# Performance work log

Hardware: AMD Instinct MI355X
Metric: run time of the kernel (lower is better)

The kernel has to match this reference:

```python
import jax, jax.numpy as jnp
import numpy as np

B, S, D, H = 4, 2048, 1024, 16
HD = D // H

def setup_inputs() -> dict:
    key = jax.random.key(0)
    ks = jax.random.split(key, 5)
    x = jax.random.normal(ks[0], (B, S, D), dtype=jnp.float32)
    mask = jnp.ones((B, S), dtype=jnp.int32)
    # torch nn.Linear init scale ~ 1/sqrt(fan_in); use small normal for stability
    qkv_w = jax.random.normal(ks[1], (3 * D, D), dtype=jnp.float32) * (1.0 / np.sqrt(D))
    qkv_b = jax.random.normal(ks[2], (3 * D,), dtype=jnp.float32) * 0.02
    out_w = jax.random.normal(ks[3], (D, D), dtype=jnp.float32) * (1.0 / np.sqrt(D))
    out_b = jax.random.normal(ks[4], (D,), dtype=jnp.float32) * 0.02
    return {"x": x, "mask": mask, "qkv_w": qkv_w, "qkv_b": qkv_b,
            "out_w": out_w, "out_b": out_b}

def reference(x, mask, qkv_w, qkv_b, out_w, out_b):
    b, s, d = x.shape
    scale = np.sqrt(HD).astype(np.float32)
    # qkv projection: torch Linear y = x @ W^T + b
    qkv = x @ qkv_w.T + qkv_b                      # (b, s, 3d)
    qkv = qkv.reshape(b, s, 3, H, HD)
    qkv = jnp.transpose(qkv, (2, 0, 3, 1, 4))      # (3, b, H, s, hd)
    q, k, v = qkv[0], qkv[1], qkv[2]
    scores = jnp.einsum('bhqd,bhkd->bhqk', q, k) / scale  # (b, H, s, s)
    neg_inf = jnp.float32(-jnp.inf)
    causal = jnp.tril(jnp.ones((s, s), dtype=bool))
    scores = jnp.where(causal[None, None], scores, neg_inf)
    key_mask = (mask != 0)[:, None, None, :]       # (b, 1, 1, s)
    scores = jnp.where(key_mask, scores, neg_inf)
    attn = jax.nn.softmax(scores, axis=-1)
    out = jnp.einsum('bhqk,bhkd->bhqd', attn, v)   # (b, H, s, hd)
    out = jnp.transpose(out, (0, 2, 1, 3)).reshape(b, s, d)
    return out @ out_w.T + out_b
```

## Files before the change

### kernel.cpp

```cpp
#include <hip/hip_runtime.h>
#include <stdint.h>
#include <type_traits>

#define BB  4
#define SS  2048
#define DD  1024
#define HH  16
#define HDD 64

typedef __attribute__((ext_vector_type(8))) short s16x8;
typedef __attribute__((ext_vector_type(4))) float f32x4;

__device__ inline short f2bf(float f) {
    union { float f; unsigned int u; } v; v.f = f;
    unsigned int r = (v.u + 0x7fffu + ((v.u >> 16) & 1u)) >> 16;
    return (short)r;
}

__device__ inline float bf2f(short s) {
    union { unsigned int u; float f; } v;
    v.u = ((unsigned int)(unsigned short)s) << 16;
    return v.f;
}

#define GLL(gp, lp) __builtin_amdgcn_global_load_lds( \
    (const __attribute__((address_space(1))) void*)(gp), \
    (__attribute__((address_space(3))) void*)(lp), 16, 0, 0)

__device__ inline void lds_barrier() {
    asm volatile("s_waitcnt lgkmcnt(0)" ::: "memory");
    __builtin_amdgcn_sched_barrier(0);
    __builtin_amdgcn_s_barrier();
    __builtin_amdgcn_sched_barrier(0);
}

__global__ void cvt_kernel(const float* __restrict__ src, short* __restrict__ dst, int n) {
    int i = (blockIdx.x * 256 + threadIdx.x) * 8;
    if (i >= n) return;
    const float4* s = (const float4*)(src + i);
    float4 a = s[0], b = s[1];
    s16x8 o;
    o[0]=f2bf(a.x); o[1]=f2bf(a.y); o[2]=f2bf(a.z); o[3]=f2bf(a.w);
    o[4]=f2bf(b.x); o[5]=f2bf(b.y); o[6]=f2bf(b.z); o[7]=f2bf(b.w);
    *(s16x8*)(dst + i) = o;
}

template<int EPI>
__global__ __launch_bounds__(256)
void gemm_bt(const short* __restrict__ A, const short* __restrict__ Bw,
             const float* __restrict__ bias, float* __restrict__ Cf,
             short* __restrict__ Qo, short* __restrict__ Ko, short* __restrict__ Vo,
             int M, int N, int K)
{
    __shared__ short lsA[128 * 32];
    __shared__ short lsB[128 * 32];
    const int tid  = threadIdx.x;
    const int w    = tid >> 6, lane = tid & 63;
    const int quad = lane >> 4, l15 = lane & 15;
    const int m0 = blockIdx.x * 128, n0 = blockIdx.y * 128;
    const int mw = (w & 1) * 64, nw = (w >> 1) * 64;

    f32x4 acc[4][4] = {};

    const int srow = w * 32 + (lane >> 2);
    const int scol = (lane & 3) * 8;
    const short* pA = A + (size_t)(m0 + srow) * K + scol;
    const short* pB = Bw + (size_t)(n0 + srow) * K + scol;
    short* lAbase0 = &lsA[(w * 32) * 32];
    short* lAbase1 = &lsA[(w * 32 + 16) * 32];
    short* lBbase0 = &lsB[(w * 32) * 32];
    short* lBbase1 = &lsB[(w * 32 + 16) * 32];

    for (int kk = 0; kk < K; kk += 32) {
        __syncthreads();
        GLL(pA + kk,            lAbase0);
        GLL(pA + kk + 16 * K,   lAbase1);
        GLL(pB + kk,            lBbase0);
        GLL(pB + kk + 16 * K,   lBbase1);
        asm volatile("s_waitcnt vmcnt(0)" ::: "memory");
        __syncthreads();

        s16x8 af[4], bfr[4];
        for (int t = 0; t < 4; ++t) {
            af[t]  = *(const s16x8*)&lsA[(mw + t * 16 + l15) * 32 + quad * 8];
            bfr[t] = *(const s16x8*)&lsB[(nw + t * 16 + l15) * 32 + quad * 8];
        }
        for (int i = 0; i < 4; ++i)
            for (int j = 0; j < 4; ++j)
                acc[i][j] = __builtin_amdgcn_mfma_f32_16x16x32_bf16(af[i], bfr[j], acc[i][j], 0, 0, 0);
    }

    if (EPI == 0) {
        for (int i = 0; i < 4; ++i) {
            int row = m0 + mw + i * 16 + quad * 4;
            for (int j = 0; j < 4; ++j) {
                int col = n0 + nw + j * 16 + l15;
                float bv = bias[col];
                for (int r = 0; r < 4; ++r)
                    Cf[(size_t)(row + r) * N + col] = acc[i][j][r] + bv;
            }
        }
    } else {
        for (int i = 0; i < 4; ++i) {
            int row = m0 + mw + i * 16 + quad * 4;
            for (int j = 0; j < 4; ++j) {
                int col = n0 + nw + j * 16 + l15;
                float bv = bias[col];
                int sel = col >> 10, h = (col >> 6) & 15, hd = col & 63;
                for (int r = 0; r < 4; ++r) {
                    int rr = row + r;
                    int b = rr >> 11, s = rr & 2047;
                    short val = f2bf(acc[i][j][r] + bv);
                    if (sel == 0)      Qo[(((size_t)b * HH + h) * SS + s) * HDD + hd] = val;
                    else if (sel == 1) Ko[(((size_t)b * HH + h) * SS + s) * HDD + hd] = val;
                    else               Vo[(((size_t)b * HH + h) * HDD + hd) * SS + s] = val;
                }
            }
        }
    }
}

__global__ __launch_bounds__(256, 4)
void attn_kernel(const short* __restrict__ Q, const short* __restrict__ Kb,
                 const short* __restrict__ Vb, const int* __restrict__ mask,
                 short* __restrict__ O)
{
    __shared__ short lsK[2][64 * 64];
    __shared__ short lsV[2][64 * 64];
    __shared__ short lsM[SS];

    const int tid  = threadIdx.x;
    const int w    = tid >> 6, lane = tid & 63;
    const int quad = lane >> 4, l15 = lane & 15;
    const int bx = blockIdx.x, bh = blockIdx.y;
    const int b = bh >> 4;
    const size_t baseQK = (size_t)bh * SS * HDD;
    const size_t baseV  = (size_t)bh * HDD * SS;
    const float SC = 0.18033688f;
    const int grow = lane >> 3;
    const int gcol = ((lane & 7) ^ grow) * 8;
    const int l7 = l15 & 7;

    {
        const int4* mp = (const int4*)(mask + b * SS);
        int4 a = mp[tid * 2], c = mp[tid * 2 + 1];
        const short NEG = f2bf(-1e30f);
        s16x8 mo;
        mo[0] = a.x ? (short)0 : NEG; mo[1] = a.y ? (short)0 : NEG;
        mo[2] = a.z ? (short)0 : NEG; mo[3] = a.w ? (short)0 : NEG;
        mo[4] = c.x ? (short)0 : NEG; mo[5] = c.y ? (short)0 : NEG;
        mo[6] = c.z ? (short)0 : NEG; mo[7] = c.w ? (short)0 : NEG;
        *(s16x8*)&lsM[tid * 8] = mo;
    }

    auto issue = [&](int kv0, int buf) {
#pragma unroll
        for (int jj = 0; jj < 2; ++jj) {
            int row = w * 16 + jj * 8 + grow;
            GLL(Kb + baseQK + (size_t)(kv0 + row) * HDD + gcol,
                &lsK[buf][(w * 2 + jj) * 512]);
        }
#pragma unroll
        for (int jj = 0; jj < 2; ++jj) {
            int row = w * 16 + jj * 8 + grow;
            GLL(Vb + baseV + (size_t)row * SS + kv0 + gcol,
                &lsV[buf][(w * 2 + jj) * 512]);
        }
    };

    for (int t = 0; t < 2; ++t) {
        const int qb = t ? bx : (31 - bx);
        const int q0 = qb * 64;
        const int qrow = q0 + w * 16 + l15;
        const int rowg0 = q0 + w * 16 + quad * 4;

        s16x8 aq[2];
#pragma unroll
        for (int ks = 0; ks < 2; ++ks)
            aq[ks] = *(const s16x8*)(Q + baseQK + (size_t)qrow * HDD + ks * 32 + quad * 8);

        float m_r[4], l_r[4];
        f32x4 o_acc[4] = {};
#pragma unroll
        for (int r = 0; r < 4; ++r) { m_r[r] = -1e30f; l_r[r] = 0.f; }

        const int ntiles = qb + 1;

        lds_barrier();
        issue(0, 0);

        auto tile = [&](auto CC, int kv0, int buf, int kvn) {
            constexpr bool CAUS = decltype(CC)::value;

            lds_barrier();
            if (kvn >= 0) issue(kvn, buf ^ 1);

            float madd[4];
#pragma unroll
            for (int nt = 0; nt < 4; ++nt)
                madd[nt] = bf2f(lsM[kv0 + nt * 16 + l15]);

            if (kvn >= 0) asm volatile("s_waitcnt vmcnt(4)" ::: "memory");
            else          asm volatile("s_waitcnt vmcnt(0)" ::: "memory");
            __builtin_amdgcn_sched_barrier(0);
            __builtin_amdgcn_s_barrier();
            __builtin_amdgcn_sched_barrier(0);

            f32x4 sv[4];
#pragma unroll
            for (int nt = 0; nt < 4; ++nt) sv[nt] = f32x4{};
#pragma unroll
            for (int ks = 0; ks < 2; ++ks)
#pragma unroll
                for (int nt = 0; nt < 4; ++nt) {
                    s16x8 kf = *(const s16x8*)&lsK[buf][(nt * 16 + l15) * 64 +
                                                       (((ks * 4 + quad) ^ l7) * 8)];
                    sv[nt] = __builtin_amdgcn_mfma_f32_16x16x32_bf16(aq[ks], kf, sv[nt], 0, 0, 0);
                }

#pragma unroll
            for (int nt = 0; nt < 4; ++nt) {
                int colg = kv0 + nt * 16 + l15;
#pragma unroll
                for (int r = 0; r < 4; ++r) {
                    float scv = sv[nt][r] * SC + madd[nt];
                    if (CAUS && colg > rowg0 + r) scv = -1e30f;
                    sv[nt][r] = scv;
                }
            }
            float alpha[4];
#pragma unroll
            for (int r = 0; r < 4; ++r) {
                float rm = fmaxf(fmaxf(sv[0][r], sv[1][r]), fmaxf(sv[2][r], sv[3][r]));
                rm = fmaxf(rm, __shfl_xor(rm, 1));
                rm = fmaxf(rm, __shfl_xor(rm, 2));
                rm = fmaxf(rm, __shfl_xor(rm, 4));
                rm = fmaxf(rm, __shfl_xor(rm, 8));
                float nm = fmaxf(m_r[r], rm);
                alpha[r] = __builtin_amdgcn_exp2f(m_r[r] - nm);
                m_r[r] = nm;
                float rs = 0.f;
#pragma unroll
                for (int nt = 0; nt < 4; ++nt) {
                    float p = __builtin_amdgcn_exp2f(sv[nt][r] - nm);
                    sv[nt][r] = p;
                    rs += p;
                }
                rs += __shfl_xor(rs, 1);
                rs += __shfl_xor(rs, 2);
                rs += __shfl_xor(rs, 4);
                rs += __shfl_xor(rs, 8);
                l_r[r] = l_r[r] * alpha[r] + rs;
            }
#pragma unroll
            for (int ht = 0; ht < 4; ++ht)
#pragma unroll
                for (int r = 0; r < 4; ++r)
                    o_acc[ht][r] *= alpha[r];

            lds_barrier();

            short* lsPw = &lsK[buf][w * 1024];
#pragma unroll
            for (int nt = 0; nt < 4; ++nt)
#pragma unroll
                for (int r = 0; r < 4; ++r) {
                    int prow = quad * 4 + r;
                    lsPw[prow * 64 + (((nt * 2 + (l15 >> 3)) ^ (prow & 7)) << 3) + l7]
                        = f2bf(sv[nt][r]);
                }
            asm volatile("s_waitcnt lgkmcnt(0)" ::: "memory");
            __builtin_amdgcn_sched_barrier(0);

            s16x8 ap[2];
#pragma unroll
            for (int k2 = 0; k2 < 2; ++k2)
                ap[k2] = *(const s16x8*)&lsPw[l15 * 64 + (((k2 * 4 + quad) ^ l7) << 3)];
#pragma unroll
            for (int ht = 0; ht < 4; ++ht)
#pragma unroll
                for (int k2 = 0; k2 < 2; ++k2) {
                    s16x8 vf = *(const s16x8*)&lsV[buf][(ht * 16 + l15) * 64 +
                                                        (((k2 * 4 + quad) ^ l7) * 8)];
                    o_acc[ht] = __builtin_amdgcn_mfma_f32_16x16x32_bf16(ap[k2], vf, o_acc[ht], 0, 0, 0);
                }
        };

        for (int kt = 0; kt < ntiles; ++kt) {
            const int kvn = (kt + 1 < ntiles) ? (kt + 1) * 64 : -1;
            if (kt == ntiles - 1) tile(std::true_type{},  kt * 64, kt & 1, kvn);
            else                  tile(std::false_type{}, kt * 64, kt & 1, kvn);
        }

        const int hcol = (bh & 15) * HDD;
#pragma unroll
        for (int r = 0; r < 4; ++r) {
            float inv = 1.0f / l_r[r];
            int srow = q0 + w * 16 + quad * 4 + r;
            size_t base = ((size_t)b * SS + srow) * DD + hcol;
#pragma unroll
            for (int ht = 0; ht < 4; ++ht)
                O[base + ht * 16 + l15] = f2bf(o_acc[ht][r] * inv);
        }
    }
}

extern "C" void kernel_launch(void* const* d_in, const int* in_sizes, int n_in,
                              void* d_out, int out_size, void* d_ws, size_t ws_size,
                              hipStream_t stream) {
    const float* x     = (const float*)d_in[0];
    const int*   mask  = (const int*)d_in[1];
    const float* qkv_w = (const float*)d_in[2];
    const float* qkv_b = (const float*)d_in[3];
    const float* out_w = (const float*)d_in[4];
    const float* out_b = (const float*)d_in[5];
    float* out = (float*)d_out;

    const size_t M1 = (size_t)BB * SS;
    short* ws  = (short*)d_ws;
    short* xb  = ws;
    short* qwb = xb  + M1 * DD;
    short* owb = qwb + (size_t)3 * DD * DD;
    short* Qb  = owb + (size_t)DD * DD;
    short* Kb  = Qb  + M1 * DD;
    short* Vb  = Kb  + M1 * DD;
    short* Ob  = Vb  + M1 * DD;

    cvt_kernel<<<(int)(M1 * DD / 8 / 256), 256, 0, stream>>>(x, xb, (int)(M1 * DD));
    cvt_kernel<<<3 * DD * DD / 8 / 256, 256, 0, stream>>>(qkv_w, qwb, 3 * DD * DD);
    cvt_kernel<<<DD * DD / 8 / 256, 256, 0, stream>>>(out_w, owb, DD * DD);

    gemm_bt<1><<<dim3(64, 24), 256, 0, stream>>>(xb, qwb, qkv_b, nullptr,
                                                 Qb, Kb, Vb, 8192, 3072, 1024);
    attn_kernel<<<dim3(16, BB * HH), 256, 0, stream>>>(Qb, Kb, Vb, mask, Ob);
    gemm_bt<0><<<dim3(64, 8), 256, 0, stream>>>(Ob, owb, out_b, out,
                                                nullptr, nullptr, nullptr, 8192, 1024, 1024);
}
```

Baseline: 350.7 us.

## Enlarge attention query tile to 128 rows with lazy softmax rescaling

```diff
diff --git a/kernel.cpp b/kernel.cpp
--- a/kernel.cpp
+++ b/kernel.cpp
@@ -120,13 +120,14 @@
     }
 }
 
-__global__ __launch_bounds__(256, 4)
+__global__ __launch_bounds__(256, 2)
 void attn_kernel(const short* __restrict__ Q, const short* __restrict__ Kb,
                  const short* __restrict__ Vb, const int* __restrict__ mask,
                  short* __restrict__ O)
 {
     __shared__ short lsK[2][64 * 64];
     __shared__ short lsV[2][64 * 64];
+    __shared__ short lsP[4][32 * 64];
     __shared__ short lsM[SS];
 
     const int tid  = threadIdx.x;
@@ -169,22 +170,26 @@
     };
 
     for (int t = 0; t < 2; ++t) {
-        const int qb = t ? bx : (31 - bx);
-        const int q0 = qb * 64;
-        const int qrow = q0 + w * 16 + l15;
-        const int rowg0 = q0 + w * 16 + quad * 4;
-
-        s16x8 aq[2];
-#pragma unroll
-        for (int ks = 0; ks < 2; ++ks)
-            aq[ks] = *(const s16x8*)(Q + baseQK + (size_t)qrow * HDD + ks * 32 + quad * 8);
-
-        float m_r[4], l_r[4];
-        f32x4 o_acc[4] = {};
-#pragma unroll
-        for (int r = 0; r < 4; ++r) { m_r[r] = -1e30f; l_r[r] = 0.f; }
-
-        const int ntiles = qb + 1;
+        const int qb = t ? bx : (15 - bx);
+        const int q0 = qb * 128;
+        const int qw0 = q0 + w * 32;
+
+        s16x8 aq[2][2];
+#pragma unroll
+        for (int s = 0; s < 2; ++s)
+#pragma unroll
+            for (int ks = 0; ks < 2; ++ks)
+                aq[s][ks] = *(const s16x8*)(Q + baseQK +
+                    (size_t)(qw0 + s * 16 + l15) * HDD + ks * 32 + quad * 8);
+
+        float m_r[2][4], l_r[2][4];
+        f32x4 o_acc[2][4] = {};
+#pragma unroll
+        for (int s = 0; s < 2; ++s)
+#pragma unroll
+            for (int r = 0; r < 4; ++r) { m_r[s][r] = -1e30f; l_r[s][r] = 0.f; }
+
+        const int ntiles = 2 * qb + 2;
 
         lds_barrier();
         issue(0, 0);
@@ -206,102 +211,142 @@
             __builtin_amdgcn_s_barrier();
             __builtin_amdgcn_sched_barrier(0);
 
-            f32x4 sv[4];
-#pragma unroll
-            for (int nt = 0; nt < 4; ++nt) sv[nt] = f32x4{};
+            f32x4 sv[2][4];
+#pragma unroll
+            for (int s = 0; s < 2; ++s)
+#pragma unroll
+                for (int nt = 0; nt < 4; ++nt) sv[s][nt] = f32x4{};
 #pragma unroll
             for (int ks = 0; ks < 2; ++ks)
 #pragma unroll
                 for (int nt = 0; nt < 4; ++nt) {
                     s16x8 kf = *(const s16x8*)&lsK[buf][(nt * 16 + l15) * 64 +
                                                        (((ks * 4 + quad) ^ l7) * 8)];
-                    sv[nt] = __builtin_amdgcn_mfma_f32_16x16x32_bf16(aq[ks], kf, sv[nt], 0, 0, 0);
-                }
-
-#pragma unroll
-            for (int nt = 0; nt < 4; ++nt) {
-                int colg = kv0 + nt * 16 + l15;
+#pragma unroll
+                    for (int s = 0; s < 2; ++s)
+                        sv[s][nt] = __builtin_amdgcn_mfma_f32_16x16x32_bf16(
+                                        aq[s][ks], kf, sv[s][nt], 0, 0, 0);
+                }
+
+#pragma unroll
+            for (int s = 0; s < 2; ++s) {
+                const int rowg0 = qw0 + s * 16 + quad * 4;
+#pragma unroll
+                for (int nt = 0; nt < 4; ++nt) {
+                    int colg = kv0 + nt * 16 + l15;
+#pragma unroll
+                    for (int r = 0; r < 4; ++r) {
+                        float scv = sv[s][nt][r] * SC + madd[nt];
+                        if (CAUS && colg > rowg0 + r) scv = -1e30f;
+                        sv[s][nt][r] = scv;
+                    }
+                }
+            }
+
+            float rm[2][4];
+#pragma unroll
+            for (int s = 0; s < 2; ++s)
 #pragma unroll
                 for (int r = 0; r < 4; ++r) {
-                    float scv = sv[nt][r] * SC + madd[nt];
-                    if (CAUS && colg > rowg0 + r) scv = -1e30f;
-                    sv[nt][r] = scv;
-                }
-            }
-            float alpha[4];
-#pragma unroll
-            for (int r = 0; r < 4; ++r) {
-                float rm = fmaxf(fmaxf(sv[0][r], sv[1][r]), fmaxf(sv[2][r], sv[3][r]));
-                rm = fmaxf(rm, __shfl_xor(rm, 1));
-                rm = fmaxf(rm, __shfl_xor(rm, 2));
-                rm = fmaxf(rm, __shfl_xor(rm, 4));
-                rm = fmaxf(rm, __shfl_xor(rm, 8));
-                float nm = fmaxf(m_r[r], rm);
-                alpha[r] = __builtin_amdgcn_exp2f(m_r[r] - nm);
-                m_r[r] = nm;
-                float rs = 0.f;
-#pragma unroll
-                for (int nt = 0; nt < 4; ++nt) {
-                    float p = __builtin_amdgcn_exp2f(sv[nt][r] - nm);
-                    sv[nt][r] = p;
-                    rs += p;
-                }
-                rs += __shfl_xor(rs, 1);
-                rs += __shfl_xor(rs, 2);
-                rs += __shfl_xor(rs, 4);
-                rs += __shfl_xor(rs, 8);
-                l_r[r] = l_r[r] * alpha[r] + rs;
-            }
-#pragma unroll
-            for (int ht = 0; ht < 4; ++ht)
+                    float v = fmaxf(fmaxf(sv[s][0][r], sv[s][1][r]),
+                                    fmaxf(sv[s][2][r], sv[s][3][r]));
+                    v = fmaxf(v, __shfl_xor(v, 1));
+                    v = fmaxf(v, __shfl_xor(v, 2));
+                    v = fmaxf(v, __shfl_xor(v, 4));
+                    v = fmaxf(v, __shfl_xor(v, 8));
+                    rm[s][r] = v;
+                }
+            float need = rm[0][0] - m_r[0][0];
+#pragma unroll
+            for (int s = 0; s < 2; ++s)
 #pragma unroll
                 for (int r = 0; r < 4; ++r)
-                    o_acc[ht][r] *= alpha[r];
-
-            lds_barrier();
-
-            short* lsPw = &lsK[buf][w * 1024];
-#pragma unroll
-            for (int nt = 0; nt < 4; ++nt)
+                    need = fmaxf(need, rm[s][r] - m_r[s][r]);
+            if (!__all(need <= 8.0f)) {
+#pragma unroll
+                for (int s = 0; s < 2; ++s)
+#pragma unroll
+                    for (int r = 0; r < 4; ++r) {
+                        float nm = fmaxf(m_r[s][r], rm[s][r]);
+                        float al = __builtin_amdgcn_exp2f(m_r[s][r] - nm);
+                        m_r[s][r] = nm;
+                        l_r[s][r] *= al;
+#pragma unroll
+                        for (int ht = 0; ht < 4; ++ht)
+                            o_acc[s][ht][r] *= al;
+                    }
+            }
+#pragma unroll
+            for (int s = 0; s < 2; ++s)
 #pragma unroll
                 for (int r = 0; r < 4; ++r) {
-                    int prow = quad * 4 + r;
-                    lsPw[prow * 64 + (((nt * 2 + (l15 >> 3)) ^ (prow & 7)) << 3) + l7]
-                        = f2bf(sv[nt][r]);
-                }
+                    float rs = 0.f;
+#pragma unroll
+                    for (int nt = 0; nt < 4; ++nt) {
+                        float p = __builtin_amdgcn_exp2f(sv[s][nt][r] - m_r[s][r]);
+                        sv[s][nt][r] = p;
+                        rs += p;
+                    }
+                    l_r[s][r] += rs;
+                }
+
+            short* lsPw = lsP[w];
+#pragma unroll
+            for (int s = 0; s < 2; ++s)
+#pragma unroll
+                for (int nt = 0; nt < 4; ++nt)
+#pragma unroll
+                    for (int r = 0; r < 4; ++r) {
+                        int prow = s * 16 + quad * 4 + r;
+                        lsPw[prow * 64 + (((nt * 2 + (l15 >> 3)) ^ (prow & 7)) << 3) + l7]
+                            = f2bf(sv[s][nt][r]);
+                    }
             asm volatile("s_waitcnt lgkmcnt(0)" ::: "memory");
             __builtin_amdgcn_sched_barrier(0);
 
-            s16x8 ap[2];
-#pragma unroll
-            for (int k2 = 0; k2 < 2; ++k2)
-                ap[k2] = *(const s16x8*)&lsPw[l15 * 64 + (((k2 * 4 + quad) ^ l7) << 3)];
+            s16x8 ap[2][2];
+#pragma unroll
+            for (int s = 0; s < 2; ++s)
+#pragma unroll
+                for (int k2 = 0; k2 < 2; ++k2)
+                    ap[s][k2] = *(const s16x8*)&lsPw[(s * 16 + l15) * 64 +
+                                                     (((k2 * 4 + quad) ^ l7) << 3)];
 #pragma unroll
             for (int ht = 0; ht < 4; ++ht)
 #pragma unroll
                 for (int k2 = 0; k2 < 2; ++k2) {
                     s16x8 vf = *(const s16x8*)&lsV[buf][(ht * 16 + l15) * 64 +
                                                         (((k2 * 4 + quad) ^ l7) * 8)];
-                    o_acc[ht] = __builtin_amdgcn_mfma_f32_16x16x32_bf16(ap[k2], vf, o_acc[ht], 0, 0, 0);
+#pragma unroll
+                    for (int s = 0; s < 2; ++s)
+                        o_acc[s][ht] = __builtin_amdgcn_mfma_f32_16x16x32_bf16(
+                                           ap[s][k2], vf, o_acc[s][ht], 0, 0, 0);
                 }
         };
 
         for (int kt = 0; kt < ntiles; ++kt) {
             const int kvn = (kt + 1 < ntiles) ? (kt + 1) * 64 : -1;
-            if (kt == ntiles - 1) tile(std::true_type{},  kt * 64, kt & 1, kvn);
-            else                  tile(std::false_type{}, kt * 64, kt & 1, kvn);
+            if (kt >= 2 * qb) tile(std::true_type{},  kt * 64, kt & 1, kvn);
+            else              tile(std::false_type{}, kt * 64, kt & 1, kvn);
         }
 
         const int hcol = (bh & 15) * HDD;
 #pragma unroll
-        for (int r = 0; r < 4; ++r) {
-            float inv = 1.0f / l_r[r];
-            int srow = q0 + w * 16 + quad * 4 + r;
-            size_t base = ((size_t)b * SS + srow) * DD + hcol;
-#pragma unroll
-            for (int ht = 0; ht < 4; ++ht)
-                O[base + ht * 16 + l15] = f2bf(o_acc[ht][r] * inv);
-        }
+        for (int s = 0; s < 2; ++s)
+#pragma unroll
+            for (int r = 0; r < 4; ++r) {
+                float ls = l_r[s][r];
+                ls += __shfl_xor(ls, 1);
+                ls += __shfl_xor(ls, 2);
+                ls += __shfl_xor(ls, 4);
+                ls += __shfl_xor(ls, 8);
+                float inv = 1.0f / ls;
+                int srow = qw0 + s * 16 + quad * 4 + r;
+                size_t base = ((size_t)b * SS + srow) * DD + hcol;
+#pragma unroll
+                for (int ht = 0; ht < 4; ++ht)
+                    O[base + ht * 16 + l15] = f2bf(o_acc[s][ht][r] * inv);
+            }
     }
 }
 
@@ -332,7 +377,7 @@
 
     gemm_bt<1><<<dim3(64, 24), 256, 0, stream>>>(xb, qwb, qkv_b, nullptr,
                                                  Qb, Kb, Vb, 8192, 3072, 1024);
-    attn_kernel<<<dim3(16, BB * HH), 256, 0, stream>>>(Qb, Kb, Vb, mask, Ob);
+    attn_kernel<<<dim3(8, BB * HH), 256, 0, stream>>>(Qb, Kb, Vb, mask, Ob);
     gemm_bt<0><<<dim3(64, 8), 256, 0, stream>>>(Ob, owb, out_b, out,
                                                 nullptr, nullptr, nullptr, 8192, 1024, 1024);
 }
```

After: 309.0 us. 1.14x faster.
